# Kernel optimization log

Hardware: AMD Instinct MI355X
Metric: run time of the kernel (lower is better)

## Reference

```python
import jax, jax.numpy as jnp
import numpy as np

BATCH, SEQ, DMODEL, DHID = 4, 4096, 1024, 1024
R_MIN, R_MAX = 0.9, 0.99
MAX_PHASE = np.pi / 50  # module overrides ctor arg with pi/50
EPS = 1e-5


def setup_inputs() -> dict:
    key = jax.random.key(0)
    ks = jax.random.split(key, 8)
    # nu_init
    u1 = jax.random.uniform(ks[0], (DHID,)) * (1 - EPS) + EPS
    mag_sq = u1 * (R_MAX ** 2 - R_MIN ** 2) + R_MIN ** 2
    nu_log = jnp.log(-0.5 * jnp.log(mag_sq + EPS))
    # theta_init
    u2 = jax.random.uniform(ks[1], (DHID,)) * (1 - EPS) + EPS
    theta_log = jnp.log(MAX_PHASE * u2)
    B_re = jax.random.normal(ks[2], (DHID, DMODEL)) / np.sqrt(2 * DMODEL)
    B_im = jax.random.normal(ks[3], (DHID, DMODEL)) / np.sqrt(2 * DMODEL)
    C_re = jax.random.normal(ks[4], (DMODEL, DHID)) / np.sqrt(DHID)
    C_im = jax.random.normal(ks[5], (DMODEL, DHID)) / np.sqrt(DHID)
    D_skip = jax.random.normal(ks[6], (DMODEL,))
    inputs = jax.random.normal(ks[7], (BATCH, SEQ, DMODEL), dtype=jnp.float32)
    return {"inputs": inputs, "nu_log": nu_log, "theta_log": theta_log,
            "B_re": B_re, "B_im": B_im, "C_re": C_re, "C_im": C_im,
            "D_skip": D_skip}


def reference(inputs, nu_log, theta_log, B_re, B_im, C_re, C_im, D_skip):
    nu = jnp.exp(nu_log)
    theta = jnp.exp(theta_log)
    diag_lambda = jnp.exp(-nu + 1j * theta)            # [H] complex
    # forward recomputes gamma_log from nu_log (parameter gamma_log unused)
    gamma_log = 0.5 * jnp.log(1 - jnp.exp(-2 * jnp.exp(nu_log)) + EPS)
    B_norm = (B_re + 1j * B_im) * jnp.exp(gamma_log)[:, None]  # [H, D]
    inputs_c = inputs.astype(jnp.complex64)
    Bu = jnp.einsum('hd,btd->bth', B_norm, inputs_c)   # [B, T, H]

    def step(h, bu_t):
        h = diag_lambda * h + bu_t
        return h, h

    h0 = jnp.zeros((inputs.shape[0], diag_lambda.shape[0]), dtype=Bu.dtype)
    _, hs = jax.lax.scan(step, h0, jnp.swapaxes(Bu, 0, 1))  # [T, B, H]
    hs = jnp.swapaxes(hs, 0, 1)                              # [B, T, H]
    C_complex = C_re + 1j * C_im                              # [D, H]
    out = jnp.einsum('bth,dh->btd', hs, C_complex).real + inputs * D_skip
    return out.astype(jnp.float32)
```

## Files before the change

kernel.cpp:

```cpp
#include <hip/hip_runtime.h>


typedef __bf16 bf16x8 __attribute__((ext_vector_type(8)));
typedef float floatx4 __attribute__((ext_vector_type(4)));

__device__ __forceinline__ unsigned short f2bf(float f) {
  unsigned u = __float_as_uint(f);
  u += 0x7fffu + ((u >> 16) & 1u);
  return (unsigned short)(u >> 16);
}
__device__ __forceinline__ float bf2f(unsigned short s) {
  return __uint_as_float(((unsigned)s) << 16);
}


__global__ void prep_params(const float* __restrict__ nu_log,
                            const float* __restrict__ theta_log,
                            float* __restrict__ lam,
                            float* __restrict__ lamL,
                            float* __restrict__ gamma)
{
  int h = blockIdx.x * 256 + threadIdx.x;
  float nu = expf(nu_log[h]);
  float th = expf(theta_log[h]);
  float r = expf(-nu);
  lam[h]        = r * cosf(th);
  lam[1024 + h] = r * sinf(th);
  float rL = expf(-128.0f * nu);
  lamL[h]        = rL * cosf(128.0f * th);
  lamL[1024 + h] = rL * sinf(128.0f * th);
  gamma[h] = sqrtf(1.0f - expf(-2.0f * nu) + 1e-5f);
}

__global__ void prep_B(const float* __restrict__ B_re, const float* __restrict__ B_im,
                       const float* __restrict__ gamma, unsigned short* __restrict__ Bcat)
{
  int tid = blockIdx.x * 256 + threadIdx.x;
  int n = tid >> 10;
  int d = tid & 1023;
  int h = n & 1023;
  float v = (n < 1024 ? B_re[h * 1024 + d] : B_im[h * 1024 + d]) * gamma[h];
  Bcat[tid] = f2bf(v);
}

__global__ void prep_C(const float* __restrict__ C_re, const float* __restrict__ C_im,
                       unsigned short* __restrict__ Ccat)
{
  int tid = blockIdx.x * 256 + threadIdx.x;
  int d = tid >> 11;
  int k = tid & 2047;
  float v = (k < 1024) ? C_re[d * 1024 + k] : -C_im[d * 1024 + (k - 1024)];
  Ccat[tid] = f2bf(v);
}

__global__ void conv_inputs(const float* __restrict__ in, unsigned short* __restrict__ outb)
{
  int tid = blockIdx.x * 256 + threadIdx.x;
  float4 v = ((const float4*)in)[tid];
  unsigned lo = (unsigned)f2bf(v.x) | ((unsigned)f2bf(v.y) << 16);
  unsigned hi = (unsigned)f2bf(v.z) | ((unsigned)f2bf(v.w) << 16);
  ((uint2*)outb)[tid] = make_uint2(lo, hi);
}


#define GLDS(gp, lp) __builtin_amdgcn_global_load_lds(                        \
      (const __attribute__((address_space(1))) void*)(gp),                    \
      (__attribute__((address_space(3))) void*)(lp), 16, 0, 0)

#define STAGE(kt, buf) do {                                                   \
    const int _ko = (kt) * 32;                                                \
    GLDS(gA0 + _ko, &As[(buf)][lofs0]);                                       \
    GLDS(gA1 + _ko, &As[(buf)][lofs1]);                                       \
    GLDS(gB0 + _ko, &Bs[(buf)][lofs0]);                                       \
    GLDS(gB1 + _ko, &Bs[(buf)][lofs1]);                                       \
  } while (0)

#define GLDS_A(kt) do {                                                       \
    const int _ko = (kt) * 32;  const int _b = (kt) & 3;                      \
    GLDS(gA0 + _ko, &As[_b][lofs0]);                                          \
    GLDS(gA1 + _ko, &As[_b][lofs1]);                                          \
  } while (0)

#define GLDS_B(kt) do {                                                       \
    const int _ko = (kt) * 32;  const int _b = (kt) & 3;                      \
    GLDS(gB0 + _ko, &Bs[_b][lofs0]);                                          \
    GLDS(gB1 + _ko, &Bs[_b][lofs1]);                                          \
  } while (0)

#define RD_B(buf) do {                                                        \
    _Pragma("unroll")                                                         \
    for (int j = 0; j < 4; ++j) {                                             \
      const int r = wn * 64 + j * 16 + lm;                                    \
      bfr[j] = *reinterpret_cast<const bf16x8*>(                              \
          &Bs[(buf)][r * 32 + (q ^ ((r >> 1) & 3)) * 8]);                     \
    }                                                                         \
  } while (0)

#define RD_A(buf, i0) do {                                                    \
    _Pragma("unroll")                                                         \
    for (int i = 0; i < 4; ++i) {                                             \
      const int r = wm * 128 + ((i0) + i) * 16 + lm;                          \
      afr[(i0) + i] = *reinterpret_cast<const bf16x8*>(                       \
          &As[(buf)][r * 32 + (q ^ ((r >> 1) & 3)) * 8]);                     \
    }                                                                         \
  } while (0)

#define MFMA16(i0) do {                                                       \
    __builtin_amdgcn_s_setprio(1);                                            \
    _Pragma("unroll")                                                         \
    for (int i = 0; i < 4; ++i)                                               \
      _Pragma("unroll")                                                       \
      for (int j = 0; j < 4; ++j)                                             \
        acc[(i0) + i][j] = __builtin_amdgcn_mfma_f32_16x16x32_bf16(           \
            afr[(i0) + i], bfr[j], acc[(i0) + i][j], 0, 0, 0);                \
    __builtin_amdgcn_s_setprio(0);                                            \
  } while (0)

#define SB0() __builtin_amdgcn_sched_barrier(0)

#define VMW(n) do {                                                           \
    SB0();                                                                    \
    asm volatile("s_waitcnt vmcnt(" #n ")" ::: "memory");                     \
    SB0();                                                                    \
  } while (0)

#define LGKMC(n) do {                                                         \
    SB0();                                                                    \
    asm volatile("s_waitcnt lgkmcnt(" #n ")" ::: "memory");                   \
    SB0();                                                                    \
  } while (0)

#define BAR() do {                                                            \
    SB0();                                                                    \
    asm volatile("" ::: "memory");                                            \
    __builtin_amdgcn_s_barrier();                                             \
    asm volatile("" ::: "memory");                                            \
    SB0();                                                                    \
  } while (0)

#define BODY_FULL(kt_) do {                                                   \
    const int _cur = (kt_) & 3;                                               \
    const int _nxt = ((kt_) + 1) & 3;                                         \
    RD_A(_cur, 4);                    \
    GLDS_A((kt_) + 3);                                                        \
    LGKMC(4);                                 \
    MFMA16(0);                                \
    LGKMC(0);                            \
    MFMA16(4);                                \
    RD_B(_nxt);                              \
    RD_A(_nxt, 0);                                                            \
    GLDS_B((kt_) + 3);                                                        \
    VMW(4);                                            \
    BAR();                                                                    \
  } while (0)

#define BODY_NOSTAGE(kt_, vm_) do {                                           \
    const int _cur = (kt_) & 3;                                               \
    const int _nxt = ((kt_) + 1) & 3;                                         \
    RD_A(_cur, 4);                                                            \
    LGKMC(4);                                                                 \
    MFMA16(0);                                                                \
    LGKMC(0);                                                                 \
    MFMA16(4);                                                                \
    RD_B(_nxt);                                                               \
    RD_A(_nxt, 0);                                                            \
    VMW(vm_);                                                                 \
    BAR();                                                                    \
  } while (0)

template <int EPI>
__global__ __launch_bounds__(512, 2) void gemm256_kernel(
    const unsigned short* __restrict__ A,
    const unsigned short* __restrict__ Bt,
    void* __restrict__ Cout,
    int M, int N, int K,
    const float* __restrict__ skip_in,
    const float* __restrict__ skip_w)
{
  __shared__ __align__(16) unsigned short As[4][256 * 32];
  __shared__ __align__(16) unsigned short Bs[4][256 * 32];

  const int tid  = threadIdx.x;
  const int lane = tid & 63;
  const int wave = tid >> 6;
  const int wm = wave >> 2;
  const int wn = wave & 3;

  const int flat    = blockIdx.x;
  const int xcd     = flat & 7;
  const int local   = flat >> 3;
  const int m_tile  = xcd * 8 + (local & 7);
  const int n_tile  = local >> 3;
  const int m0 = m_tile * 256;
  const int n0 = n_tile * 256;

  const int ldr = lane >> 2;
  const int pos = lane & 3;
  const int lm  = lane & 15;
  const int q   = lane >> 4;

  const int r0 = wave * 32 + ldr;
  const int r1 = r0 + 16;
  const int ca0 = pos ^ ((r0 >> 1) & 3);
  const int ca1 = pos ^ ((r1 >> 1) & 3);

  const unsigned short* gA0 = A  + (size_t)(m0 + r0) * K + ca0 * 8;
  const unsigned short* gA1 = A  + (size_t)(m0 + r1) * K + ca1 * 8;
  const unsigned short* gB0 = Bt + (size_t)(n0 + r0) * K + ca0 * 8;
  const unsigned short* gB1 = Bt + (size_t)(n0 + r1) * K + ca1 * 8;
  const int lofs0 = r0 * 32 + pos * 8;
  const int lofs1 = r1 * 32 + pos * 8;

  floatx4 acc[8][4];
#pragma unroll
  for (int i = 0; i < 8; ++i)
#pragma unroll
    for (int j = 0; j < 4; ++j)
      acc[i][j] = (floatx4){0.f, 0.f, 0.f, 0.f};

  const int KT = K >> 5;

  bf16x8 afr[8], bfr[4];

  STAGE(0, 0);
  STAGE(1, 1);
  STAGE(2, 2);
  VMW(4);
  BAR();
  RD_B(0);
  RD_A(0, 0);

  for (int kt = 0; kt + 3 < KT; ++kt)
    BODY_FULL(kt);

  BODY_NOSTAGE(KT - 3, 0);
  BODY_NOSTAGE(KT - 2, 0);
  {
    const int _cur = (KT - 1) & 3;
    RD_A(_cur, 4);
    LGKMC(4);
    MFMA16(0);
    LGKMC(0);
    MFMA16(4);
  }

#pragma unroll
  for (int i = 0; i < 8; ++i) {
#pragma unroll
    for (int j = 0; j < 4; ++j) {
      const int row0 = m0 + wm * 128 + i * 16 + q * 4;
      const int col  = n0 + wn * 64 + j * 16 + lm;
#pragma unroll
      for (int r = 0; r < 4; ++r) {
        const size_t idx = (size_t)(row0 + r) * N + col;
        if (EPI == 0) {
          ((unsigned short*)Cout)[idx] = f2bf(acc[i][j][r]);
        } else {
          ((float*)Cout)[idx] = acc[i][j][r] + skip_in[idx] * skip_w[col];
        }
      }
    }
  }
}


__global__ void scan_finals(const unsigned short* __restrict__ Bu,
                            const float* __restrict__ lam,
                            float2* __restrict__ finals)
{
  int tid = blockIdx.x * 256 + threadIdx.x;
  int h = tid & 1023, c = (tid >> 10) & 31, b = tid >> 15;
  float lre = lam[h], lim = lam[1024 + h];
  const unsigned short* p = Bu + ((size_t)(b * 4096 + c * 128) * 2048) + h;
  float yre = 0.f, yim = 0.f;
#pragma unroll 4
  for (int t = 0; t < 128; ++t) {
    float ure = bf2f(p[0]);
    float uim = bf2f(p[1024]);
    float nre = fmaf(lre, yre, fmaf(-lim, yim, ure));
    float nim = fmaf(lre, yim, fmaf(lim, yre, uim));
    yre = nre; yim = nim;
    p += 2048;
  }
  finals[tid] = make_float2(yre, yim);
}

__global__ void scan_carries(const float2* __restrict__ finals,
                             const float* __restrict__ lamL,
                             float2* __restrict__ carry)
{
  int tid = blockIdx.x * 256 + threadIdx.x;
  int h = tid & 1023, b = tid >> 10;
  float Lre = lamL[h], Lim = lamL[1024 + h];
  float Hre = 0.f, Him = 0.f;
  for (int c = 0; c < 32; ++c) {
    size_t i = ((size_t)(b * 32 + c) << 10) + h;
    carry[i] = make_float2(Hre, Him);
    float2 f = finals[i];
    float nre = fmaf(Lre, Hre, fmaf(-Lim, Him, f.x));
    float nim = fmaf(Lre, Him, fmaf(Lim, Hre, f.y));
    Hre = nre; Him = nim;
  }
}

__global__ void scan_apply(const float* __restrict__ lam,
                           const float2* __restrict__ carry,
                           unsigned short* __restrict__ Bu)
{
  int tid = blockIdx.x * 256 + threadIdx.x;
  int h = tid & 1023, c = (tid >> 10) & 31, b = tid >> 15;
  float lre = lam[h], lim = lam[1024 + h];
  float2 cv = carry[tid];
  float yre = cv.x, yim = cv.y;
  unsigned short* p = Bu + ((size_t)(b * 4096 + c * 128) * 2048) + h;
#pragma unroll 4
  for (int t = 0; t < 128; ++t) {
    float ure = bf2f(p[0]);
    float uim = bf2f(p[1024]);
    float nre = fmaf(lre, yre, fmaf(-lim, yim, ure));
    float nim = fmaf(lre, yim, fmaf(lim, yre, uim));
    yre = nre; yim = nim;
    p[0]    = f2bf(yre);
    p[1024] = f2bf(yim);
    p += 2048;
  }
}


extern "C" void kernel_launch(void* const* d_in, const int* in_sizes, int n_in,
                              void* d_out, int out_size, void* d_ws, size_t ws_size,
                              hipStream_t stream)
{
  const float* inputs    = (const float*)d_in[0];
  const float* nu_log    = (const float*)d_in[1];
  const float* theta_log = (const float*)d_in[2];
  const float* B_re      = (const float*)d_in[3];
  const float* B_im      = (const float*)d_in[4];
  const float* C_re      = (const float*)d_in[5];
  const float* C_im      = (const float*)d_in[6];
  const float* D_skip    = (const float*)d_in[7];
  float* out = (float*)d_out;

  char* ws = (char*)d_ws;
  float* lam   = (float*)ws;
  float* lamL  = lam + 2048;
  float* gamma = lamL + 2048;
  unsigned short* inp_bf = (unsigned short*)(ws + (1 << 16));
  unsigned short* Bcat   = inp_bf + (size_t)16384 * 1024;
  unsigned short* Ccat   = Bcat   + (size_t)2048 * 1024;
  unsigned short* Bu     = Ccat   + (size_t)1024 * 2048;
  float2* finals = (float2*)(Bu + (size_t)16384 * 2048);
  float2* carry  = finals + 131072;

  prep_params<<<4,    256, 0, stream>>>(nu_log, theta_log, lam, lamL, gamma);
  prep_B     <<<8192, 256, 0, stream>>>(B_re, B_im, gamma, Bcat);
  prep_C     <<<8192, 256, 0, stream>>>(C_re, C_im, Ccat);
  conv_inputs<<<16384,256, 0, stream>>>(inputs, inp_bf);

  gemm256_kernel<0><<<512, 512, 0, stream>>>(
      inp_bf, Bcat, Bu, 16384, 2048, 1024, nullptr, nullptr);

  scan_finals <<<512, 256, 0, stream>>>(Bu, lam, finals);
  scan_carries<<<16,  256, 0, stream>>>(finals, lamL, carry);
  scan_apply  <<<512, 256, 0, stream>>>(lam, carry, Bu);

  gemm256_kernel<1><<<256, 512, 0, stream>>>(
      Bu, Ccat, out, 16384, 1024, 2048, inputs, D_skip);
}
```

Measured before the change: 319.6 us.

## Shrink GEMM tile to 256x128 with double buffering and vectorize chunked scan

```diff
diff --git a/kernel.cpp b/kernel.cpp
--- a/kernel.cpp
+++ b/kernel.cpp
@@ -26,9 +26,9 @@
   float r = expf(-nu);
   lam[h]        = r * cosf(th);
   lam[1024 + h] = r * sinf(th);
-  float rL = expf(-128.0f * nu);
-  lamL[h]        = rL * cosf(128.0f * th);
-  lamL[1024 + h] = rL * sinf(128.0f * th);
+  float rL = expf(-64.0f * nu);
+  lamL[h]        = rL * cosf(64.0f * th);
+  lamL[1024 + h] = rL * sinf(64.0f * th);
   gamma[h] = sqrtf(1.0f - expf(-2.0f * nu) + 1e-5f);
 }
 
@@ -67,41 +67,31 @@
       (const __attribute__((address_space(1))) void*)(gp),                    \
       (__attribute__((address_space(3))) void*)(lp), 16, 0, 0)
 
-#define STAGE(kt, buf) do {                                                   \
+#define STAGE6(kt, S) do {                                                    \
     const int _ko = (kt) * 32;                                                \
-    GLDS(gA0 + _ko, &As[(buf)][lofs0]);                                       \
-    GLDS(gA1 + _ko, &As[(buf)][lofs1]);                                       \
-    GLDS(gB0 + _ko, &Bs[(buf)][lofs0]);                                       \
-    GLDS(gB1 + _ko, &Bs[(buf)][lofs1]);                                       \
-  } while (0)
-
-#define GLDS_A(kt) do {                                                       \
-    const int _ko = (kt) * 32;  const int _b = (kt) & 3;                      \
-    GLDS(gA0 + _ko, &As[_b][lofs0]);                                          \
-    GLDS(gA1 + _ko, &As[_b][lofs1]);                                          \
-  } while (0)
-
-#define GLDS_B(kt) do {                                                       \
-    const int _ko = (kt) * 32;  const int _b = (kt) & 3;                      \
-    GLDS(gB0 + _ko, &Bs[_b][lofs0]);                                          \
-    GLDS(gB1 + _ko, &Bs[_b][lofs1]);                                          \
-  } while (0)
-
-#define RD_B(buf) do {                                                        \
+    GLDS(gA0 + _ko, &As[(S)][dA0]);                                           \
+    GLDS(gA1 + _ko, &As[(S)][dA1]);                                           \
+    GLDS(gA2 + _ko, &As[(S)][dA2]);                                           \
+    GLDS(gA3 + _ko, &As[(S)][dA3]);                                           \
+    GLDS(gB0 + _ko, &Bs[(S)][dB0]);                                           \
+    GLDS(gB1 + _ko, &Bs[(S)][dB1]);                                           \
+  } while (0)
+
+#define RD_B(S) do {                                                          \
     _Pragma("unroll")                                                         \
     for (int j = 0; j < 4; ++j) {                                             \
       const int r = wn * 64 + j * 16 + lm;                                    \
       bfr[j] = *reinterpret_cast<const bf16x8*>(                              \
-          &Bs[(buf)][r * 32 + (q ^ ((r >> 1) & 3)) * 8]);                     \
+          &Bs[(S)][r * 32 + (q ^ ((r >> 1) & 3)) * 8]);                       \
     }                                                                         \
   } while (0)
 
-#define RD_A(buf, i0) do {                                                    \
+#define RD_A(S, i0) do {                                                      \
     _Pragma("unroll")                                                         \
     for (int i = 0; i < 4; ++i) {                                             \
       const int r = wm * 128 + ((i0) + i) * 16 + lm;                          \
       afr[(i0) + i] = *reinterpret_cast<const bf16x8*>(                       \
-          &As[(buf)][r * 32 + (q ^ ((r >> 1) & 3)) * 8]);                     \
+          &As[(S)][r * 32 + (q ^ ((r >> 1) & 3)) * 8]);                       \
     }                                                                         \
   } while (0)
 
@@ -118,9 +108,9 @@
 
 #define SB0() __builtin_amdgcn_sched_barrier(0)
 
-#define VMW(n) do {                                                           \
-    SB0();                                                                    \
-    asm volatile("s_waitcnt vmcnt(" #n ")" ::: "memory");                     \
+#define VMW0() do {                                                           \
+    SB0();                                                                    \
+    asm volatile("s_waitcnt vmcnt(0)" ::: "memory");                          \
     SB0();                                                                    \
   } while (0)
 
@@ -138,38 +128,21 @@
     SB0();                                                                    \
   } while (0)
 
-#define BODY_FULL(kt_) do {                                                   \
-    const int _cur = (kt_) & 3;                                               \
-    const int _nxt = ((kt_) + 1) & 3;                                         \
-    RD_A(_cur, 4);                    \
-    GLDS_A((kt_) + 3);                                                        \
-    LGKMC(4);                                 \
-    MFMA16(0);                                \
+#define BODY(kt_, C, N) do {                                                  \
+    STAGE6((kt_) + 1, N);                                                     \
+    RD_A(C, 4);                                                               \
+    LGKMC(4);                       \
+    MFMA16(0);                                                                \
     LGKMC(0);                            \
-    MFMA16(4);                                \
-    RD_B(_nxt);                              \
-    RD_A(_nxt, 0);                                                            \
-    GLDS_B((kt_) + 3);                                                        \
-    VMW(4);                                            \
-    BAR();                                                                    \
-  } while (0)
-
-#define BODY_NOSTAGE(kt_, vm_) do {                                           \
-    const int _cur = (kt_) & 3;                                               \
-    const int _nxt = ((kt_) + 1) & 3;                                         \
-    RD_A(_cur, 4);                                                            \
-    LGKMC(4);                                                                 \
-    MFMA16(0);                                                                \
-    LGKMC(0);                                                                 \
     MFMA16(4);                                                                \
-    RD_B(_nxt);                                                               \
-    RD_A(_nxt, 0);                                                            \
-    VMW(vm_);                                                                 \
-    BAR();                                                                    \
+    VMW0();              \
+    BAR();                                   \
+    RD_B(N);                                                                  \
+    RD_A(N, 0);             \
   } while (0)
 
 template <int EPI>
-__global__ __launch_bounds__(512, 2) void gemm256_kernel(
+__global__ __launch_bounds__(256) void gemm256_kernel(
     const unsigned short* __restrict__ A,
     const unsigned short* __restrict__ Bt,
     void* __restrict__ Cout,
@@ -177,14 +150,14 @@
     const float* __restrict__ skip_in,
     const float* __restrict__ skip_w)
 {
-  __shared__ __align__(16) unsigned short As[4][256 * 32];
-  __shared__ __align__(16) unsigned short Bs[4][256 * 32];
+  __shared__ __align__(16) unsigned short As[2][256 * 32];
+  __shared__ __align__(16) unsigned short Bs[2][128 * 32];
 
   const int tid  = threadIdx.x;
   const int lane = tid & 63;
   const int wave = tid >> 6;
-  const int wm = wave >> 2;
-  const int wn = wave & 3;
+  const int wm = wave >> 1;
+  const int wn = wave & 1;
 
   const int flat    = blockIdx.x;
   const int xcd     = flat & 7;
@@ -192,24 +165,29 @@
   const int m_tile  = xcd * 8 + (local & 7);
   const int n_tile  = local >> 3;
   const int m0 = m_tile * 256;
-  const int n0 = n_tile * 256;
+  const int n0 = n_tile * 128;
 
   const int ldr = lane >> 2;
   const int pos = lane & 3;
   const int lm  = lane & 15;
   const int q   = lane >> 4;
 
-  const int r0 = wave * 32 + ldr;
-  const int r1 = r0 + 16;
-  const int ca0 = pos ^ ((r0 >> 1) & 3);
-  const int ca1 = pos ^ ((r1 >> 1) & 3);
-
-  const unsigned short* gA0 = A  + (size_t)(m0 + r0) * K + ca0 * 8;
-  const unsigned short* gA1 = A  + (size_t)(m0 + r1) * K + ca1 * 8;
-  const unsigned short* gB0 = Bt + (size_t)(n0 + r0) * K + ca0 * 8;
-  const unsigned short* gB1 = Bt + (size_t)(n0 + r1) * K + ca1 * 8;
-  const int lofs0 = r0 * 32 + pos * 8;
-  const int lofs1 = r1 * 32 + pos * 8;
+  const int rs = wave * 16 + ldr;
+  const int rA0 = rs,      rA1 = rs + 64, rA2 = rs + 128, rA3 = rs + 192;
+  const int rB0 = rs,      rB1 = rs + 64;
+  const int cA0 = pos ^ ((rA0 >> 1) & 3), cA1 = pos ^ ((rA1 >> 1) & 3);
+  const int cA2 = pos ^ ((rA2 >> 1) & 3), cA3 = pos ^ ((rA3 >> 1) & 3);
+  const int cB0 = pos ^ ((rB0 >> 1) & 3), cB1 = pos ^ ((rB1 >> 1) & 3);
+
+  const unsigned short* gA0 = A  + (size_t)(m0 + rA0) * K + cA0 * 8;
+  const unsigned short* gA1 = A  + (size_t)(m0 + rA1) * K + cA1 * 8;
+  const unsigned short* gA2 = A  + (size_t)(m0 + rA2) * K + cA2 * 8;
+  const unsigned short* gA3 = A  + (size_t)(m0 + rA3) * K + cA3 * 8;
+  const unsigned short* gB0 = Bt + (size_t)(n0 + rB0) * K + cB0 * 8;
+  const unsigned short* gB1 = Bt + (size_t)(n0 + rB1) * K + cB1 * 8;
+  const int dA0 = rA0 * 32 + pos * 8, dA1 = rA1 * 32 + pos * 8;
+  const int dA2 = rA2 * 32 + pos * 8, dA3 = rA3 * 32 + pos * 8;
+  const int dB0 = rB0 * 32 + pos * 8, dB1 = rB1 * 32 + pos * 8;
 
   floatx4 acc[8][4];
 #pragma unroll
@@ -222,22 +200,19 @@
 
   bf16x8 afr[8], bfr[4];
 
-  STAGE(0, 0);
-  STAGE(1, 1);
-  STAGE(2, 2);
-  VMW(4);
+  STAGE6(0, 0);
+  VMW0();
   BAR();
   RD_B(0);
   RD_A(0, 0);
 
-  for (int kt = 0; kt + 3 < KT; ++kt)
-    BODY_FULL(kt);
-
-  BODY_NOSTAGE(KT - 3, 0);
-  BODY_NOSTAGE(KT - 2, 0);
+  for (int kt = 0; kt + 2 < KT; kt += 2) {
+    BODY(kt,     0, 1);
+    BODY(kt + 1, 1, 0);
+  }
+  BODY(KT - 2, 0, 1);
   {
-    const int _cur = (KT - 1) & 3;
-    RD_A(_cur, 4);
+    RD_A(1, 4);
     LGKMC(4);
     MFMA16(0);
     LGKMC(0);
@@ -266,62 +241,78 @@
 
 __global__ void scan_finals(const unsigned short* __restrict__ Bu,
                             const float* __restrict__ lam,
-                            float2* __restrict__ finals)
-{
-  int tid = blockIdx.x * 256 + threadIdx.x;
-  int h = tid & 1023, c = (tid >> 10) & 31, b = tid >> 15;
-  float lre = lam[h], lim = lam[1024 + h];
-  const unsigned short* p = Bu + ((size_t)(b * 4096 + c * 128) * 2048) + h;
-  float yre = 0.f, yim = 0.f;
+                            float4* __restrict__ finals4)
+{
+  int tid = blockIdx.x * 256 + threadIdx.x;
+  int h2 = tid & 511, c = (tid >> 9) & 63, b = tid >> 15;
+  int h0 = h2 * 2;
+  float2 lre = *(const float2*)&lam[h0];
+  float2 lim = *(const float2*)&lam[1024 + h0];
+  const unsigned short* p = Bu + ((size_t)(b * 4096 + c * 64) * 2048) + h0;
+  float y0re = 0.f, y0im = 0.f, y1re = 0.f, y1im = 0.f;
 #pragma unroll 4
-  for (int t = 0; t < 128; ++t) {
-    float ure = bf2f(p[0]);
-    float uim = bf2f(p[1024]);
-    float nre = fmaf(lre, yre, fmaf(-lim, yim, ure));
-    float nim = fmaf(lre, yim, fmaf(lim, yre, uim));
-    yre = nre; yim = nim;
+  for (int t = 0; t < 64; ++t) {
+    unsigned ure = *(const unsigned*)(p);
+    unsigned uim = *(const unsigned*)(p + 1024);
+    float u0re = bf2f((unsigned short)ure), u1re = bf2f((unsigned short)(ure >> 16));
+    float u0im = bf2f((unsigned short)uim), u1im = bf2f((unsigned short)(uim >> 16));
+    float n0re = fmaf(lre.x, y0re, fmaf(-lim.x, y0im, u0re));
+    float n0im = fmaf(lre.x, y0im, fmaf(lim.x, y0re, u0im));
+    float n1re = fmaf(lre.y, y1re, fmaf(-lim.y, y1im, u1re));
+    float n1im = fmaf(lre.y, y1im, fmaf(lim.y, y1re, u1im));
+    y0re = n0re; y0im = n0im; y1re = n1re; y1im = n1im;
     p += 2048;
   }
-  finals[tid] = make_float2(yre, yim);
-}
-
-__global__ void scan_carries(const float2* __restrict__ finals,
+  finals4[tid] = make_float4(y0re, y0im, y1re, y1im);
+}
+
+__global__ void scan_carries(const float4* __restrict__ finals4,
                              const float* __restrict__ lamL,
-                             float2* __restrict__ carry)
-{
-  int tid = blockIdx.x * 256 + threadIdx.x;
-  int h = tid & 1023, b = tid >> 10;
-  float Lre = lamL[h], Lim = lamL[1024 + h];
-  float Hre = 0.f, Him = 0.f;
-  for (int c = 0; c < 32; ++c) {
-    size_t i = ((size_t)(b * 32 + c) << 10) + h;
-    carry[i] = make_float2(Hre, Him);
-    float2 f = finals[i];
-    float nre = fmaf(Lre, Hre, fmaf(-Lim, Him, f.x));
-    float nim = fmaf(Lre, Him, fmaf(Lim, Hre, f.y));
-    Hre = nre; Him = nim;
+                             float4* __restrict__ carry4)
+{
+  int tid = blockIdx.x * 256 + threadIdx.x;
+  int h2 = tid & 511, b = tid >> 9;
+  int h0 = h2 * 2;
+  float2 Lre = *(const float2*)&lamL[h0];
+  float2 Lim = *(const float2*)&lamL[1024 + h0];
+  float H0re = 0.f, H0im = 0.f, H1re = 0.f, H1im = 0.f;
+  for (int c = 0; c < 64; ++c) {
+    size_t i = ((size_t)(b * 64 + c) << 9) + h2;
+    carry4[i] = make_float4(H0re, H0im, H1re, H1im);
+    float4 f = finals4[i];
+    float n0re = fmaf(Lre.x, H0re, fmaf(-Lim.x, H0im, f.x));
+    float n0im = fmaf(Lre.x, H0im, fmaf(Lim.x, H0re, f.y));
+    float n1re = fmaf(Lre.y, H1re, fmaf(-Lim.y, H1im, f.z));
+    float n1im = fmaf(Lre.y, H1im, fmaf(Lim.y, H1re, f.w));
+    H0re = n0re; H0im = n0im; H1re = n1re; H1im = n1im;
   }
 }
 
 __global__ void scan_apply(const float* __restrict__ lam,
-                           const float2* __restrict__ carry,
+                           const float4* __restrict__ carry4,
                            unsigned short* __restrict__ Bu)
 {
   int tid = blockIdx.x * 256 + threadIdx.x;
-  int h = tid & 1023, c = (tid >> 10) & 31, b = tid >> 15;
-  float lre = lam[h], lim = lam[1024 + h];
-  float2 cv = carry[tid];
-  float yre = cv.x, yim = cv.y;
-  unsigned short* p = Bu + ((size_t)(b * 4096 + c * 128) * 2048) + h;
+  int h2 = tid & 511, c = (tid >> 9) & 63, b = tid >> 15;
+  int h0 = h2 * 2;
+  float2 lre = *(const float2*)&lam[h0];
+  float2 lim = *(const float2*)&lam[1024 + h0];
+  float4 cv = carry4[tid];
+  float y0re = cv.x, y0im = cv.y, y1re = cv.z, y1im = cv.w;
+  unsigned short* p = Bu + ((size_t)(b * 4096 + c * 64) * 2048) + h0;
 #pragma unroll 4
-  for (int t = 0; t < 128; ++t) {
-    float ure = bf2f(p[0]);
-    float uim = bf2f(p[1024]);
-    float nre = fmaf(lre, yre, fmaf(-lim, yim, ure));
-    float nim = fmaf(lre, yim, fmaf(lim, yre, uim));
-    yre = nre; yim = nim;
-    p[0]    = f2bf(yre);
-    p[1024] = f2bf(yim);
+  for (int t = 0; t < 64; ++t) {
+    unsigned ure = *(const unsigned*)(p);
+    unsigned uim = *(const unsigned*)(p + 1024);
+    float u0re = bf2f((unsigned short)ure), u1re = bf2f((unsigned short)(ure >> 16));
+    float u0im = bf2f((unsigned short)uim), u1im = bf2f((unsigned short)(uim >> 16));
+    float n0re = fmaf(lre.x, y0re, fmaf(-lim.x, y0im, u0re));
+    float n0im = fmaf(lre.x, y0im, fmaf(lim.x, y0re, u0im));
+    float n1re = fmaf(lre.y, y1re, fmaf(-lim.y, y1im, u1re));
+    float n1im = fmaf(lre.y, y1im, fmaf(lim.y, y1re, u1im));
+    y0re = n0re; y0im = n0im; y1re = n1re; y1im = n1im;
+    *(unsigned*)(p)        = (unsigned)f2bf(y0re) | ((unsigned)f2bf(y1re) << 16);
+    *(unsigned*)(p + 1024) = (unsigned)f2bf(y0im) | ((unsigned)f2bf(y1im) << 16);
     p += 2048;
   }
 }
@@ -349,21 +340,21 @@
   unsigned short* Bcat   = inp_bf + (size_t)16384 * 1024;
   unsigned short* Ccat   = Bcat   + (size_t)2048 * 1024;
   unsigned short* Bu     = Ccat   + (size_t)1024 * 2048;
-  float2* finals = (float2*)(Bu + (size_t)16384 * 2048);
-  float2* carry  = finals + 131072;
+  float4* finals4 = (float4*)(Bu + (size_t)16384 * 2048);
+  float4* carry4  = finals4 + 131072;
 
   prep_params<<<4,    256, 0, stream>>>(nu_log, theta_log, lam, lamL, gamma);
   prep_B     <<<8192, 256, 0, stream>>>(B_re, B_im, gamma, Bcat);
   prep_C     <<<8192, 256, 0, stream>>>(C_re, C_im, Ccat);
   conv_inputs<<<16384,256, 0, stream>>>(inputs, inp_bf);
 
-  gemm256_kernel<0><<<512, 512, 0, stream>>>(
+  gemm256_kernel<0><<<1024, 256, 0, stream>>>(
       inp_bf, Bcat, Bu, 16384, 2048, 1024, nullptr, nullptr);
 
-  scan_finals <<<512, 256, 0, stream>>>(Bu, lam, finals);
-  scan_carries<<<16,  256, 0, stream>>>(finals, lamL, carry);
-  scan_apply  <<<512, 256, 0, stream>>>(lam, carry, Bu);
-
-  gemm256_kernel<1><<<256, 512, 0, stream>>>(
+  scan_finals <<<512, 256, 0, stream>>>(Bu, lam, finals4);
+  scan_carries<<<8,   256, 0, stream>>>(finals4, lamL, carry4);
+  scan_apply  <<<512, 256, 0, stream>>>(lam, carry4, Bu);
+
+  gemm256_kernel<1><<<512, 256, 0, stream>>>(
       Bu, Ccat, out, 16384, 1024, 2048, inputs, D_skip);
 }
```

After: 463.4 us. +45.0%, slower.
